# Kernel optimization log

Measured on AMD Instinct MI355X. Metric: run time of the kernel, lower is better.

## Reference

```python
import jax, jax.numpy as jnp
import numpy as np
from jax import lax

SIM_RATIO = 0.5
TAU = 1e-4
BN_EPS = 1e-5
COS_EPS = 1e-6
LEAKY_SLOPE = 0.01


def setup_inputs() -> dict:
    key = jax.random.key(0)
    ks = jax.random.split(key, 4)
    B, N, D = 2048, 50000, 128
    user_item_id = jax.random.randint(ks[0], (B, 2), 0, N, dtype=jnp.int64 if jax.config.jax_enable_x64 else jnp.int32).astype(jnp.int32)
    item_feature = jax.random.normal(ks[1], (B, 2 * D), dtype=jnp.float32)
    all_items = jax.random.normal(ks[2], (N, D), dtype=jnp.float32)
    # Linear(2D -> D) params (stored transposed: x @ W + b), BatchNorm1d affine params
    W = jax.random.normal(ks[3], (2 * D, D), dtype=jnp.float32) / np.float32(np.sqrt(2 * D))
    b = jnp.zeros((D,), jnp.float32)
    gamma = jnp.ones((D,), jnp.float32)
    beta = jnp.zeros((D,), jnp.float32)
    return {"user_item_id": user_item_id, "item_feature": item_feature,
            "all_items": all_items, "W": W, "b": b, "gamma": gamma, "beta": beta}


def _mlp(x, W, b, gamma, beta):
    # Linear + BatchNorm1d (training mode: batch stats, biased var) + LeakyReLU
    h = x @ W + b                                  # [B, D]
    mean = h.mean(axis=0)
    var = ((h - mean) ** 2).mean(axis=0)
    h = (h - mean) * lax.rsqrt(var + BN_EPS) * gamma + beta
    return jnp.where(h >= 0, h, LEAKY_SLOPE * h)


def reference(user_item_id, item_feature, all_items, W, b, gamma, beta):
    B = item_feature.shape[0]
    N = all_items.shape[0]
    h = _mlp(item_feature, W, b, gamma, beta)       # [B, D]
    scores = h @ all_items.T                         # [B, N]
    # hard gumbel-softmax, tau=1e-4
    g = jax.random.gumbel(jax.random.key(42), scores.shape, scores.dtype)
    soft = jax.nn.softmax((scores + g) / TAU, axis=-1)
    idx = jnp.argmax(soft, axis=-1)                  # [B]
    onehot = jax.nn.one_hot(idx, N, dtype=scores.dtype)
    probs = onehot + soft - lax.stop_gradient(soft)  # straight-through hard one-hot
    repl_feat = probs @ all_items                    # [B, D] (one-hot gather via matmul)
    repl_items = (jnp.arange(N, dtype=scores.dtype) * probs).sum(axis=1).astype(jnp.int32)
    orig_feat = all_items[user_item_id[:, 1]]        # [B, D]
    # cosine similarity along dim=1 with eps=1e-6 (torch semantics)
    dot = (orig_feat * repl_feat).sum(axis=1)
    n1 = jnp.maximum(jnp.linalg.norm(orig_feat, axis=1), COS_EPS)
    n2 = jnp.maximum(jnp.linalg.norm(repl_feat, axis=1), COS_EPS)
    sim = dot / (n1 * n2)
    sim = (sim + 1.0) / 2.0                          # regularize_similarity
    labels = jnp.full((B,), SIM_RATIO, dtype=sim.dtype)
    sim_loss = jnp.mean((sim - labels) ** 2)         # SimilarityMarginLoss ~ MSE to ratio
    return repl_items, sim_loss, sim.mean()
```

## Files before the change

### kernel.cpp

```cpp
#include <hip/hip_runtime.h>
#include <math.h>

#define TINYF 1.17549435e-38f
#define GMAX 16.0f
#define NT16 3125
#define SPT16 49

typedef __attribute__((ext_vector_type(8))) short bf16x8;
typedef __attribute__((ext_vector_type(4))) float f32x4;

__device__ __forceinline__ unsigned rotl32(unsigned x, int r) {
  return (x << r) | (x >> (32 - r));
}

__device__ __forceinline__ unsigned tf2x32_xor(unsigned x0, unsigned x1) {
  const unsigned k0 = 0u, k1 = 42u, k2 = 0x1BD11BF0u;
  x0 += k0; x1 += k1;
#define TFR(r) { x0 += x1; x1 = rotl32(x1, r); x1 ^= x0; }
  TFR(13) TFR(15) TFR(26) TFR(6)
  x0 += k1; x1 += k2 + 1u;
  TFR(17) TFR(29) TFR(16) TFR(24)
  x0 += k2; x1 += k0 + 2u;
  TFR(13) TFR(15) TFR(26) TFR(6)
  x0 += k0; x1 += k1 + 3u;
  TFR(17) TFR(29) TFR(16) TFR(24)
  x0 += k1; x1 += k2 + 4u;
  TFR(13) TFR(15) TFR(26) TFR(6)
  x0 += k2; x1 += k0 + 5u;
#undef TFR
  return x0 ^ x1;
}

__device__ __forceinline__ float gumbel_from_bits(unsigned bits) {
  float f = __uint_as_float((bits >> 9) | 0x3f800000u) - 1.0f;
  float u = fmaxf(f, TINYF);
  return -logf(-logf(u));
}

__device__ __forceinline__ unsigned ordf(float v) {
  unsigned b = __float_as_uint(v);
  return (b & 0x80000000u) ? ~b : (b | 0x80000000u);
}
__device__ __forceinline__ float unordf(unsigned u) {
  unsigned b = (u & 0x80000000u) ? (u & 0x7FFFFFFFu) : ~u;
  return __uint_as_float(b);
}

__device__ __forceinline__ unsigned short f2bf(float f) {
  unsigned u = __float_as_uint(f);
  unsigned r = u + 0x7FFFu + ((u >> 16) & 1u);
  return (unsigned short)(r >> 16);
}
__device__ __forceinline__ unsigned pk2(float a, float b) {
  return (unsigned)f2bf(a) | ((unsigned)f2bf(b) << 16);
}
__device__ __forceinline__ int bswz(int b) { return b ^ (((b >> 8) & 7) << 4); }

__device__ __attribute__((noinline)) void resolve_cand(
    int R, int J, float s, float ERRC,
    const float* __restrict__ hfin, const float* __restrict__ items,
    const unsigned* __restrict__ V0u,
    unsigned long long* __restrict__ rowslot, const volatile unsigned* hiw) {
  const unsigned v0 = V0u[R];
  const unsigned hi0 = hiw[2 * R + 1];
  float tv = v0 ? unordf(v0) : -3.4e38f;
  if (hi0) tv = fmaxf(tv, unordf(hi0));
  const float thr2 = tv - ERRC;
  const float d = thr2 - s;
  const unsigned bits = tf2x32_xor(0u, (unsigned)R * 50000u + (unsigned)J);
  const float f = __uint_as_float((bits >> 9) | 0x3f800000u) - 1.0f;
  const float u = fmaxf(f, TINYF);
  const float thr_u = __expf(-__expf(-d)) * (1.0f - 2e-5f);
  if (u < thr_u) return;
  const float g = -logf(-logf(u));
  if (s + g < thr2) return;
  const float4* hp = (const float4*)(hfin + (size_t)R * 128);
  const float4* ap = (const float4*)(items + (size_t)J * 128);
  float4 a4 = {0.f, 0.f, 0.f, 0.f};
#pragma unroll
  for (int k = 0; k < 32; ++k) {
    float4 h = hp[k];
    float4 b = ap[k];
    a4.x = fmaf(h.x, b.x, a4.x);
    a4.y = fmaf(h.y, b.y, a4.y);
    a4.z = fmaf(h.z, b.z, a4.z);
    a4.w = fmaf(h.w, b.w, a4.w);
  }
  const float v = ((a4.x + a4.y) + (a4.z + a4.w)) + g;
  const unsigned ov = ordf(v);
  if (ov >= hiw[2 * R + 1]) {
    const unsigned long long pk =
        ((unsigned long long)ov << 32) | (0xFFFFFFFFu - (unsigned)J);
    atomicMax(&rowslot[R], pk);
  }
}

__global__ void k_pre(const float* __restrict__ x, const float* __restrict__ W,
                      const float* __restrict__ b, float* __restrict__ hraw,
                      const float* __restrict__ items,
                      unsigned short* __restrict__ ib, float* __restrict__ norms) {
  __shared__ float sx[2][256];
  __shared__ float red[4];
  const int t = threadIdx.x;
  const int bid = blockIdx.x;
  if (bid < 1024) {
    const int rr = t >> 7, d = t & 127;
    const int i = bid * 2 + rr;
    sx[rr][d] = x[i * 256 + d];
    sx[rr][d + 128] = x[i * 256 + 128 + d];
    __syncthreads();
    double acc = 0.0;
    for (int k = 0; k < 256; ++k)
      acc = fma((double)sx[rr][k], (double)W[k * 128 + d], acc);
    hraw[i * 128 + d] = (float)acc + b[d];
  } else {
    const int bb = bid - 1024;
    const int row = bb * 32 + (t >> 3);
    const int rc = row > 49999 ? 49999 : row;
    const int c = (t & 7) * 16;
    const float4* p = (const float4*)(items + (size_t)rc * 128 + c);
    const float4 v0 = p[0], v1 = p[1], v2 = p[2], v3 = p[3];
    float ss = v0.x * v0.x + v0.y * v0.y + v0.z * v0.z + v0.w * v0.w +
               v1.x * v1.x + v1.y * v1.y + v1.z * v1.z + v1.w * v1.w +
               v2.x * v2.x + v2.y * v2.y + v2.z * v2.z + v2.w * v2.w +
               v3.x * v3.x + v3.y * v3.y + v3.z * v3.z + v3.w * v3.w;
    if (row <= 49999) {
      uint4 o0, o1;
      o0.x = pk2(v0.x, v0.y); o0.y = pk2(v0.z, v0.w);
      o0.z = pk2(v1.x, v1.y); o0.w = pk2(v1.z, v1.w);
      o1.x = pk2(v2.x, v2.y); o1.y = pk2(v2.z, v2.w);
      o1.z = pk2(v3.x, v3.y); o1.w = pk2(v3.z, v3.w);
      uint4* dst = (uint4*)(ib + (size_t)row * 128 + c);
      dst[0] = o0; dst[1] = o1;
    }
    ss += __shfl_xor(ss, 1);
    ss += __shfl_xor(ss, 2);
    ss += __shfl_xor(ss, 4);
    ss = fmaxf(ss, __shfl_xor(ss, 8));
    ss = fmaxf(ss, __shfl_xor(ss, 16));
    ss = fmaxf(ss, __shfl_xor(ss, 32));
    if ((t & 63) == 0) red[t >> 6] = ss;
    __syncthreads();
    if (t == 0) {
      float mx = fmaxf(fmaxf(red[0], red[1]), fmaxf(red[2], red[3]));
      atomicMax((unsigned*)&norms[1], __float_as_uint(mx));
    }
  }
}

__global__ void k_bnstats(const float* __restrict__ hraw,
                          float* __restrict__ meanv, float* __restrict__ rsv) {
  __shared__ double red[256];
  const int d = blockIdx.x;
  const int t = threadIdx.x;
  double s = 0.0;
  for (int i = t; i < 2048; i += 256) s += (double)hraw[i * 128 + d];
  red[t] = s;
  __syncthreads();
  for (int off = 128; off > 0; off >>= 1) {
    if (t < off) red[t] += red[t + off];
    __syncthreads();
  }
  const float m = (float)(red[0] * (1.0 / 2048.0));
  __syncthreads();
  double v = 0.0;
  for (int i = t; i < 2048; i += 256) {
    float dd = __fsub_rn(hraw[i * 128 + d], m);
    v += (double)dd * (double)dd;
  }
  red[t] = v;
  __syncthreads();
  for (int off = 128; off > 0; off >>= 1) {
    if (t < off) red[t] += red[t + off];
    __syncthreads();
  }
  if (t == 0) {
    float var = (float)(red[0] * (1.0 / 2048.0));
    float vpe = __fadd_rn(var, 1e-5f);
    meanv[d] = m;
    rsv[d] = (float)(1.0 / sqrt((double)vpe));
  }
}

__global__ void k_apply(const float* __restrict__ hraw,
                        const float* __restrict__ meanv, const float* __restrict__ rsv,
                        const float* __restrict__ gamma, const float* __restrict__ beta,
                        float* __restrict__ hfin, unsigned short* __restrict__ hb,
                        float* __restrict__ norms) {
  __shared__ float red[256];
  const int t = threadIdx.x;
  const int idx = blockIdx.x * 256 + t;
  const int d = idx & 127;
  float h = hraw[idx];
  float hn = __fadd_rn(__fmul_rn(__fmul_rn(__fsub_rn(h, meanv[d]), rsv[d]), gamma[d]), beta[d]);
  float o = (hn >= 0.0f) ? hn : __fmul_rn(0.01f, hn);
  hfin[idx] = o;
  hb[idx] = f2bf(o);
  red[t] = o * o;
  __syncthreads();
  for (int off = 64; off > 0; off >>= 1) {
    if ((t & 127) < off) red[t] += red[t + off];
    __syncthreads();
  }
  if ((t & 127) == 0) atomicMax((unsigned*)&norms[0], __float_as_uint(red[t]));
}

__global__ __launch_bounds__(256, 2) void k_seed(
    const unsigned short* __restrict__ hb, const unsigned short* __restrict__ ib,
    const float* __restrict__ norms, unsigned* __restrict__ V0u) {
  const int t = threadIdx.x;
  const int w = t >> 6, l = t & 63;
  const int lg = l >> 4, lr = l & 15;
  const int rg = blockIdx.x >> 3;
  const int jspan = blockIdx.x & 7;
  const int r0w = rg * 64 + w * 16;
  const float ERRC = 0.004f * sqrtf(norms[0] * norms[1]) + 0.01f;

  const unsigned short* aB0 = hb + (size_t)(r0w + lr) * 128 + lg * 8;
  bf16x8 Afrag[4];
#pragma unroll
  for (int kb = 0; kb < 4; ++kb) Afrag[kb] = *(const bf16x8*)(aB0 + kb * 32);

  float vmax[4] = {-3.4e38f, -3.4e38f, -3.4e38f, -3.4e38f};
  for (int itr = 0; itr < 8; ++itr) {
    const int J = jspan * 128 + itr * 16 + lr;
    const unsigned short* bp = ib + (size_t)J * 128 + lg * 8;
    f32x4 acc = (f32x4){0.f, 0.f, 0.f, 0.f};
#pragma unroll
    for (int kb = 0; kb < 4; ++kb)
      acc = __builtin_amdgcn_mfma_f32_16x16x32_bf16(Afrag[kb], *(const bf16x8*)(bp + kb * 32), acc, 0, 0, 0);
#pragma unroll
    for (int q = 0; q < 4; ++q) {
      const int R = r0w + lg * 4 + q;
      const float g = gumbel_from_bits(tf2x32_xor(0u, (unsigned)R * 50000u + (unsigned)J));
      vmax[q] = fmaxf(vmax[q], acc[q] + g);
    }
  }
#pragma unroll
  for (int m = 1; m <= 8; m <<= 1)
#pragma unroll
    for (int q = 0; q < 4; ++q) vmax[q] = fmaxf(vmax[q], __shfl_xor(vmax[q], m));
  if (lr == 0) {
#pragma unroll
    for (int q = 0; q < 4; ++q)
      atomicMax(&V0u[r0w + lg * 4 + q], ordf(vmax[q] - ERRC));
  }
}

__global__ __launch_bounds__(256, 2) void k_screen(
    const unsigned short* __restrict__ hb, const float* __restrict__ hfin,
    const float* __restrict__ items, const unsigned short* __restrict__ ib,
    const unsigned* __restrict__ V0u,
    const float* __restrict__ norms, unsigned long long* __restrict__ rowslot) {
  __shared__ __align__(16) unsigned short Bs[4][2][16 * 128];
  __shared__ unsigned qk[4][128];
  __shared__ float qsh[4][128];

  const int t = threadIdx.x;
  const int w = t >> 6, l = t & 63;
  const int lg = l >> 4, lr = l & 15;
  const int rg = blockIdx.x >> 6;
  const int span = blockIdx.x & 63;
  const int r0w = rg * 128 + w * 32;
  const int tile0 = span * SPT16;
  int nt = NT16 - tile0;
  nt = nt < 0 ? 0 : (nt > SPT16 ? SPT16 : nt);
  if (nt == 0) return;

  const float ERRC = 0.004f * sqrtf(norms[0] * norms[1]) + 0.01f;
  const volatile unsigned* hiw = (const volatile unsigned*)rowslot;

  const unsigned short* aB0 = hb + (size_t)(r0w + lr) * 128 + lg * 8;
  bf16x8 Afrag[2][4];
#pragma unroll
  for (int kb = 0; kb < 4; ++kb) {
    Afrag[0][kb] = *(const bf16x8*)(aB0 + kb * 32);
    Afrag[1][kb] = *(const bf16x8*)(aB0 + 16 * 128 + kb * 32);
  }

  char* wlds = (char*)Bs + w * 8192;
  const char* ibc = (const char*)ib;
  int so[4];
#pragma unroll
  for (int c = 0; c < 4; ++c) {
    const int row = c * 4 + (l >> 4);
    const int col = (l & 15) * 16;
    so[c] = row * 256 + (col ^ ((row & 7) << 4));
  }

#define ISSUE(tl, pbuf)                                                        \
  {                                                                            \
    const char* gs = ibc + (size_t)(tl) * 4096;                                \
    char* ld = wlds + (pbuf) * 4096;                                           \
    __builtin_amdgcn_global_load_lds((const unsigned*)(gs + so[0]),            \
                                     (unsigned*)(ld), 16, 0, 0);               \
    __builtin_amdgcn_global_load_lds((const unsigned*)(gs + so[1]),            \
                                     (unsigned*)(ld + 1024), 16, 0, 0);        \
    __builtin_amdgcn_global_load_lds((const unsigned*)(gs + so[2]),            \
                                     (unsigned*)(ld + 2048), 16, 0, 0);        \
    __builtin_amdgcn_global_load_lds((const unsigned*)(gs + so[3]),            \
                                     (unsigned*)(ld + 3072), 16, 0, 0);        \
  }
#define WAITVM4() { asm volatile("s_waitcnt vmcnt(4)" ::: "memory"); \
                    __builtin_amdgcn_sched_barrier(0); }
#define WAITVM0() { asm volatile("s_waitcnt vmcnt(0)" ::: "memory"); \
                    __builtin_amdgcn_sched_barrier(0); }

  ISSUE(tile0, 0)

  const unsigned long long lml = (1ull << l) - 1ull;
  unsigned qn = 0;
  float th1[2][4];

  int pb = 0;
  for (int it = 0; it < nt; ++it) {
    const int j0 = (tile0 + it) * 16;

    if (it + 1 < nt) {
      ISSUE(tile0 + it + 1, pb ^ 1)
      WAITVM4()
    } else {
      WAITVM0()
    }

    if ((it & 7) == 0) {
      float tvl = -3.4e38f;
      if (l < 32) {
        const int R = r0w + l;
        const unsigned v0 = V0u[R];
        if (v0) tvl = unordf(v0);
        const unsigned hi = hiw[2 * R + 1];
        if (hi) tvl = fmaxf(tvl, unordf(hi));
      }
#pragma unroll
      for (int rt = 0; rt < 2; ++rt)
#pragma unroll
        for (int q = 0; q < 4; ++q)
          th1[rt][q] = __shfl(tvl, rt * 16 + lg * 4 + q) - GMAX - ERRC;
    }

    f32x4 p0 = (f32x4){0.f, 0.f, 0.f, 0.f};
    f32x4 p1 = (f32x4){0.f, 0.f, 0.f, 0.f};
    f32x4 q0 = (f32x4){0.f, 0.f, 0.f, 0.f};
    f32x4 q1 = (f32x4){0.f, 0.f, 0.f, 0.f};
    const char* tb = wlds + pb * 4096;
    {
      bf16x8 b0 = *(const bf16x8*)(tb + bswz(lr * 256 + 0 * 64 + lg * 16));
      bf16x8 b1 = *(const bf16x8*)(tb + bswz(lr * 256 + 1 * 64 + lg * 16));
      bf16x8 b2 = *(const bf16x8*)(tb + bswz(lr * 256 + 2 * 64 + lg * 16));
      bf16x8 b3 = *(const bf16x8*)(tb + bswz(lr * 256 + 3 * 64 + lg * 16));
      p0 = __builtin_amdgcn_mfma_f32_16x16x32_bf16(Afrag[0][0], b0, p0, 0, 0, 0);
      q0 = __builtin_amdgcn_mfma_f32_16x16x32_bf16(Afrag[1][0], b0, q0, 0, 0, 0);
      p1 = __builtin_amdgcn_mfma_f32_16x16x32_bf16(Afrag[0][1], b1, p1, 0, 0, 0);
      q1 = __builtin_amdgcn_mfma_f32_16x16x32_bf16(Afrag[1][1], b1, q1, 0, 0, 0);
      p0 = __builtin_amdgcn_mfma_f32_16x16x32_bf16(Afrag[0][2], b2, p0, 0, 0, 0);
      q0 = __builtin_amdgcn_mfma_f32_16x16x32_bf16(Afrag[1][2], b2, q0, 0, 0, 0);
      p1 = __builtin_amdgcn_mfma_f32_16x16x32_bf16(Afrag[0][3], b3, p1, 0, 0, 0);
      q1 = __builtin_amdgcn_mfma_f32_16x16x32_bf16(Afrag[1][3], b3, q1, 0, 0, 0);
    }
    const f32x4 acc0 = p0 + p1;
    const f32x4 acc1 = q0 + q1;

#pragma unroll
    for (int rt = 0; rt < 2; ++rt)
#pragma unroll
      for (int q = 0; q < 4; ++q) {
        const float s = rt ? acc1[q] : acc0[q];
        const int J = j0 + lr;
        const bool c = (s >= th1[rt][q]);
        const unsigned long long m = __ballot(c);
        if (m) {
          if (c) {
            const unsigned idx = qn + (unsigned)__popcll(m & lml);
            qk[w][idx] = ((unsigned)(rt * 16 + lg * 4 + q) << 16) | (unsigned)J;
            qsh[w][idx] = s;
          }
          qn += (unsigned)__popcll(m);
          if (qn >= 64) {
            for (unsigned i = (unsigned)l; i < qn; i += 64) {
              const unsigned key = qk[w][i];
              resolve_cand(r0w + (int)(key >> 16), (int)(key & 0xFFFFu),
                           qsh[w][i], ERRC, hfin, items, V0u, rowslot, hiw);
            }
            qn = 0;
          }
        }
      }

    pb ^= 1;
  }

  for (unsigned i = (unsigned)l; i < qn; i += 64) {
    const unsigned key = qk[w][i];
    resolve_cand(r0w + (int)(key >> 16), (int)(key & 0xFFFFu),
                 qsh[w][i], ERRC, hfin, items, V0u, rowslot, hiw);
  }
#undef ISSUE
#undef WAITVM4
#undef WAITVM0
}

__global__ void k_final(const unsigned long long* __restrict__ rowslot,
                        const int* __restrict__ uid, const float* __restrict__ items,
                        float* __restrict__ dout, float* __restrict__ simv) {
  const int r = blockIdx.x;
  const int lane = threadIdx.x;
  const unsigned long long pk = rowslot[r];
  const int bi = (int)(0xFFFFFFFFu - (unsigned)pk);
  if (lane == 0) dout[r] = (float)bi;

  const int orig = uid[r * 2 + 1];
  float o1 = items[(size_t)orig * 128 + lane];
  float o2 = items[(size_t)orig * 128 + 64 + lane];
  float p1 = items[(size_t)bi * 128 + lane];
  float p2 = items[(size_t)bi * 128 + 64 + lane];
  float d = o1 * p1 + o2 * p2;
  float s1 = o1 * o1 + o2 * o2;
  float s2 = p1 * p1 + p2 * p2;
  for (int off = 32; off > 0; off >>= 1) {
    d += __shfl_down(d, off);
    s1 += __shfl_down(s1, off);
    s2 += __shfl_down(s2, off);
  }
  if (lane == 0) {
    float n1 = fmaxf(sqrtf(s1), 1e-6f);
    float n2 = fmaxf(sqrtf(s2), 1e-6f);
    float sim = d / (n1 * n2);
    simv[r] = (sim + 1.0f) * 0.5f;
  }
}

__global__ void k_reduce(const float* __restrict__ simv, float* __restrict__ dout) {
  __shared__ double rl[256];
  __shared__ double rs[256];
  const int t = threadIdx.x;
  double L = 0.0, S = 0.0;
  for (int i = t; i < 2048; i += 256) {
    double s = (double)simv[i];
    double dd = s - 0.5;
    L += dd * dd;
    S += s;
  }
  rl[t] = L; rs[t] = S;
  __syncthreads();
  for (int off = 128; off > 0; off >>= 1) {
    if (t < off) { rl[t] += rl[t + off]; rs[t] += rs[t + off]; }
    __syncthreads();
  }
  if (t == 0) {
    dout[2048] = (float)(rl[0] * (1.0 / 2048.0));
    dout[2049] = (float)(rs[0] * (1.0 / 2048.0));
  }
}

extern "C" void kernel_launch(void* const* d_in, const int* in_sizes, int n_in,
                              void* d_out, int out_size, void* d_ws, size_t ws_size,
                              hipStream_t stream) {
  const int* uid = (const int*)d_in[0];
  const float* xfeat = (const float*)d_in[1];
  const float* items = (const float*)d_in[2];
  const float* W = (const float*)d_in[3];
  const float* bias = (const float*)d_in[4];
  const float* gamma = (const float*)d_in[5];
  const float* beta = (const float*)d_in[6];

  float* ws = (float*)d_ws;
  float* hraw = ws;
  float* hfin = ws + 262144;
  float* meanv = ws + 524288;
  float* rsv = ws + 524416;
  unsigned* V0u = (unsigned*)(ws + 524544);
  float* simv = ws + 526592;
  float* norms = ws + 528640;
  unsigned long long* rowslot =
      (unsigned long long*)(ws + 528642);
  unsigned short* hb = (unsigned short*)(ws + 532740);
  unsigned short* ib = (unsigned short*)(ws + 663812);
  float* dout = (float*)d_out;

  hipMemsetAsync(V0u, 0, 2048 * 4, stream);
  hipMemsetAsync(norms, 0, 8 + 2048 * 8, stream);

  hipLaunchKernelGGL(k_pre, dim3(2587), dim3(256), 0, stream, xfeat, W, bias, hraw, items, ib, norms);
  hipLaunchKernelGGL(k_bnstats, dim3(128), dim3(256), 0, stream, hraw, meanv, rsv);
  hipLaunchKernelGGL(k_apply, dim3(1024), dim3(256), 0, stream, hraw, meanv, rsv, gamma, beta, hfin, hb, norms);
  hipLaunchKernelGGL(k_seed, dim3(256), dim3(256), 0, stream, hb, ib, norms, V0u);
  hipLaunchKernelGGL(k_screen, dim3(1024), dim3(256), 0, stream, hb, hfin, items, ib, V0u, norms, rowslot);
  hipLaunchKernelGGL(k_final, dim3(2048), dim3(64), 0, stream, rowslot, uid, items, dout, simv);
  hipLaunchKernelGGL(k_reduce, dim3(1), dim3(256), 0, stream, simv, dout);
}
```

Measured before the change: 335.9 us.

## Load item tiles directly to registers, double grid, fuse final reduction

The screening kernel drops its LDS double buffer fed by global_load_lds and instead prefetches the next item tile straight into registers, which removes the LDS traffic and swizzle math. The item range is split into twice as many spans, doubling the grid for better load balance across CUs. The separate single-block reduction kernel is removed: k_final accumulates the loss and mean with double atomics, and the last block writes the outputs. Risks include higher register pressure, less coalesced global loads, and atomic contention on two doubles.

```diff
diff --git a/kernel.cpp b/kernel.cpp
--- a/kernel.cpp
+++ b/kernel.cpp
@@ -4,7 +4,7 @@
 #define TINYF 1.17549435e-38f
 #define GMAX 16.0f
 #define NT16 3125
-#define SPT16 49
+#define SPT 25
 
 typedef __attribute__((ext_vector_type(8))) short bf16x8;
 typedef __attribute__((ext_vector_type(4))) float f32x4;
@@ -54,7 +54,6 @@
 __device__ __forceinline__ unsigned pk2(float a, float b) {
   return (unsigned)f2bf(a) | ((unsigned)f2bf(b) << 16);
 }
-__device__ __forceinline__ int bswz(int b) { return b ^ (((b >> 8) & 7) << 4); }
 
 __device__ __attribute__((noinline)) void resolve_cand(
     int R, int J, float s, float ERRC,
@@ -252,19 +251,18 @@
     const float* __restrict__ items, const unsigned short* __restrict__ ib,
     const unsigned* __restrict__ V0u,
     const float* __restrict__ norms, unsigned long long* __restrict__ rowslot) {
-  __shared__ __align__(16) unsigned short Bs[4][2][16 * 128];
   __shared__ unsigned qk[4][128];
   __shared__ float qsh[4][128];
 
   const int t = threadIdx.x;
   const int w = t >> 6, l = t & 63;
   const int lg = l >> 4, lr = l & 15;
-  const int rg = blockIdx.x >> 6;
-  const int span = blockIdx.x & 63;
+  const int rg = blockIdx.x >> 7;
+  const int span = blockIdx.x & 127;
   const int r0w = rg * 128 + w * 32;
-  const int tile0 = span * SPT16;
+  const int tile0 = span * SPT;
   int nt = NT16 - tile0;
-  nt = nt < 0 ? 0 : (nt > SPT16 ? SPT16 : nt);
+  nt = nt < 0 ? 0 : (nt > SPT ? SPT : nt);
   if (nt == 0) return;
 
   const float ERRC = 0.004f * sqrtf(norms[0] * norms[1]) + 0.01f;
@@ -278,49 +276,23 @@
     Afrag[1][kb] = *(const bf16x8*)(aB0 + 16 * 128 + kb * 32);
   }
 
-  char* wlds = (char*)Bs + w * 8192;
-  const char* ibc = (const char*)ib;
-  int so[4];
-#pragma unroll
-  for (int c = 0; c < 4; ++c) {
-    const int row = c * 4 + (l >> 4);
-    const int col = (l & 15) * 16;
-    so[c] = row * 256 + (col ^ ((row & 7) << 4));
-  }
-
-#define ISSUE(tl, pbuf)                                                        \
-  {                                                                            \
-    const char* gs = ibc + (size_t)(tl) * 4096;                                \
-    char* ld = wlds + (pbuf) * 4096;                                           \
-    __builtin_amdgcn_global_load_lds((const unsigned*)(gs + so[0]),            \
-                                     (unsigned*)(ld), 16, 0, 0);               \
-    __builtin_amdgcn_global_load_lds((const unsigned*)(gs + so[1]),            \
-                                     (unsigned*)(ld + 1024), 16, 0, 0);        \
-    __builtin_amdgcn_global_load_lds((const unsigned*)(gs + so[2]),            \
-                                     (unsigned*)(ld + 2048), 16, 0, 0);        \
-    __builtin_amdgcn_global_load_lds((const unsigned*)(gs + so[3]),            \
-                                     (unsigned*)(ld + 3072), 16, 0, 0);        \
-  }
-#define WAITVM4() { asm volatile("s_waitcnt vmcnt(4)" ::: "memory"); \
-                    __builtin_amdgcn_sched_barrier(0); }
-#define WAITVM0() { asm volatile("s_waitcnt vmcnt(0)" ::: "memory"); \
-                    __builtin_amdgcn_sched_barrier(0); }
-
-  ISSUE(tile0, 0)
+  const unsigned short* bptr = ib + (size_t)(tile0 * 16 + lr) * 128 + lg * 8;
+
+  bf16x8 cur[4], nxt[4];
+#pragma unroll
+  for (int kb = 0; kb < 4; ++kb) cur[kb] = *(const bf16x8*)(bptr + kb * 32);
 
   const unsigned long long lml = (1ull << l) - 1ull;
   unsigned qn = 0;
   float th1[2][4];
 
-  int pb = 0;
   for (int it = 0; it < nt; ++it) {
     const int j0 = (tile0 + it) * 16;
 
     if (it + 1 < nt) {
-      ISSUE(tile0 + it + 1, pb ^ 1)
-      WAITVM4()
-    } else {
-      WAITVM0()
+      const unsigned short* nbp = bptr + (size_t)(it + 1) * 2048;
+#pragma unroll
+      for (int kb = 0; kb < 4; ++kb) nxt[kb] = *(const bf16x8*)(nbp + kb * 32);
     }
 
     if ((it & 7) == 0) {
@@ -343,21 +315,14 @@
     f32x4 p1 = (f32x4){0.f, 0.f, 0.f, 0.f};
     f32x4 q0 = (f32x4){0.f, 0.f, 0.f, 0.f};
     f32x4 q1 = (f32x4){0.f, 0.f, 0.f, 0.f};
-    const char* tb = wlds + pb * 4096;
-    {
-      bf16x8 b0 = *(const bf16x8*)(tb + bswz(lr * 256 + 0 * 64 + lg * 16));
-      bf16x8 b1 = *(const bf16x8*)(tb + bswz(lr * 256 + 1 * 64 + lg * 16));
-      bf16x8 b2 = *(const bf16x8*)(tb + bswz(lr * 256 + 2 * 64 + lg * 16));
-      bf16x8 b3 = *(const bf16x8*)(tb + bswz(lr * 256 + 3 * 64 + lg * 16));
-      p0 = __builtin_amdgcn_mfma_f32_16x16x32_bf16(Afrag[0][0], b0, p0, 0, 0, 0);
-      q0 = __builtin_amdgcn_mfma_f32_16x16x32_bf16(Afrag[1][0], b0, q0, 0, 0, 0);
-      p1 = __builtin_amdgcn_mfma_f32_16x16x32_bf16(Afrag[0][1], b1, p1, 0, 0, 0);
-      q1 = __builtin_amdgcn_mfma_f32_16x16x32_bf16(Afrag[1][1], b1, q1, 0, 0, 0);
-      p0 = __builtin_amdgcn_mfma_f32_16x16x32_bf16(Afrag[0][2], b2, p0, 0, 0, 0);
-      q0 = __builtin_amdgcn_mfma_f32_16x16x32_bf16(Afrag[1][2], b2, q0, 0, 0, 0);
-      p1 = __builtin_amdgcn_mfma_f32_16x16x32_bf16(Afrag[0][3], b3, p1, 0, 0, 0);
-      q1 = __builtin_amdgcn_mfma_f32_16x16x32_bf16(Afrag[1][3], b3, q1, 0, 0, 0);
-    }
+    p0 = __builtin_amdgcn_mfma_f32_16x16x32_bf16(Afrag[0][0], cur[0], p0, 0, 0, 0);
+    q0 = __builtin_amdgcn_mfma_f32_16x16x32_bf16(Afrag[1][0], cur[0], q0, 0, 0, 0);
+    p1 = __builtin_amdgcn_mfma_f32_16x16x32_bf16(Afrag[0][1], cur[1], p1, 0, 0, 0);
+    q1 = __builtin_amdgcn_mfma_f32_16x16x32_bf16(Afrag[1][1], cur[1], q1, 0, 0, 0);
+    p0 = __builtin_amdgcn_mfma_f32_16x16x32_bf16(Afrag[0][2], cur[2], p0, 0, 0, 0);
+    q0 = __builtin_amdgcn_mfma_f32_16x16x32_bf16(Afrag[1][2], cur[2], q0, 0, 0, 0);
+    p1 = __builtin_amdgcn_mfma_f32_16x16x32_bf16(Afrag[0][3], cur[3], p1, 0, 0, 0);
+    q1 = __builtin_amdgcn_mfma_f32_16x16x32_bf16(Afrag[1][3], cur[3], q1, 0, 0, 0);
     const f32x4 acc0 = p0 + p1;
     const f32x4 acc1 = q0 + q1;
 
@@ -387,7 +352,8 @@
         }
       }
 
-    pb ^= 1;
+#pragma unroll
+    for (int kb = 0; kb < 4; ++kb) cur[kb] = nxt[kb];
   }
 
   for (unsigned i = (unsigned)l; i < qn; i += 64) {
@@ -395,14 +361,12 @@
     resolve_cand(r0w + (int)(key >> 16), (int)(key & 0xFFFFu),
                  qsh[w][i], ERRC, hfin, items, V0u, rowslot, hiw);
   }
-#undef ISSUE
-#undef WAITVM4
-#undef WAITVM0
 }
 
 __global__ void k_final(const unsigned long long* __restrict__ rowslot,
                         const int* __restrict__ uid, const float* __restrict__ items,
-                        float* __restrict__ dout, float* __restrict__ simv) {
+                        float* __restrict__ dout, double* __restrict__ accLS,
+                        unsigned* __restrict__ done) {
   const int r = blockIdx.x;
   const int lane = threadIdx.x;
   const unsigned long long pk = rowslot[r];
@@ -426,30 +390,18 @@
     float n1 = fmaxf(sqrtf(s1), 1e-6f);
     float n2 = fmaxf(sqrtf(s2), 1e-6f);
     float sim = d / (n1 * n2);
-    simv[r] = (sim + 1.0f) * 0.5f;
-  }
-}
-
-__global__ void k_reduce(const float* __restrict__ simv, float* __restrict__ dout) {
-  __shared__ double rl[256];
-  __shared__ double rs[256];
-  const int t = threadIdx.x;
-  double L = 0.0, S = 0.0;
-  for (int i = t; i < 2048; i += 256) {
-    double s = (double)simv[i];
-    double dd = s - 0.5;
-    L += dd * dd;
-    S += s;
-  }
-  rl[t] = L; rs[t] = S;
-  __syncthreads();
-  for (int off = 128; off > 0; off >>= 1) {
-    if (t < off) { rl[t] += rl[t + off]; rs[t] += rs[t + off]; }
-    __syncthreads();
-  }
-  if (t == 0) {
-    dout[2048] = (float)(rl[0] * (1.0 / 2048.0));
-    dout[2049] = (float)(rs[0] * (1.0 / 2048.0));
+    sim = (sim + 1.0f) * 0.5f;
+    const double s = (double)sim;
+    const double dd = s - 0.5;
+    atomicAdd(&accLS[0], dd * dd);
+    atomicAdd(&accLS[1], s);
+    __threadfence();
+    const unsigned old = atomicAdd(done, 1u);
+    if (old == 2047u) {
+      __threadfence();
+      dout[2048] = (float)(accLS[0] * (1.0 / 2048.0));
+      dout[2049] = (float)(accLS[1] * (1.0 / 2048.0));
+    }
   }
 }
 
@@ -470,7 +422,8 @@
   float* meanv = ws + 524288;
   float* rsv = ws + 524416;
   unsigned* V0u = (unsigned*)(ws + 524544);
-  float* simv = ws + 526592;
+  double* accLS = (double*)(ws + 526592);
+  unsigned* done = (unsigned*)(ws + 526596);
   float* norms = ws + 528640;
   unsigned long long* rowslot =
       (unsigned long long*)(ws + 528642);
@@ -478,14 +431,13 @@
   unsigned short* ib = (unsigned short*)(ws + 663812);
   float* dout = (float*)d_out;
 
-  hipMemsetAsync(V0u, 0, 2048 * 4, stream);
+  hipMemsetAsync(V0u, 0, 2048 * 4 + 24, stream);
   hipMemsetAsync(norms, 0, 8 + 2048 * 8, stream);
 
   hipLaunchKernelGGL(k_pre, dim3(2587), dim3(256), 0, stream, xfeat, W, bias, hraw, items, ib, norms);
   hipLaunchKernelGGL(k_bnstats, dim3(128), dim3(256), 0, stream, hraw, meanv, rsv);
   hipLaunchKernelGGL(k_apply, dim3(1024), dim3(256), 0, stream, hraw, meanv, rsv, gamma, beta, hfin, hb, norms);
   hipLaunchKernelGGL(k_seed, dim3(256), dim3(256), 0, stream, hb, ib, norms, V0u);
-  hipLaunchKernelGGL(k_screen, dim3(1024), dim3(256), 0, stream, hb, hfin, items, ib, V0u, norms, rowslot);
-  hipLaunchKernelGGL(k_final, dim3(2048), dim3(64), 0, stream, rowslot, uid, items, dout, simv);
-  hipLaunchKernelGGL(k_reduce, dim3(1), dim3(256), 0, stream, simv, dout);
-}
+  hipLaunchKernelGGL(k_screen, dim3(2048), dim3(256), 0, stream, hb, hfin, items, ib, V0u, norms, rowslot);
+  hipLaunchKernelGGL(k_final, dim3(2048), dim3(64), 0, stream, rowslot, uid, items, dout, accLS, done);
+}
```

New measurement: 472.0 us. 1.41x slower.
